# Performance work log

Measured on AMD Instinct MI355X. Metric: run time of the kernel, lower is better.

## Reference

```python
import jax, jax.numpy as jnp
import numpy as np

T, B, D, H, A = 256, 512, 128, 128, 8
RUN_COUNT = 1000

def _orth(k, shape, scale):
    w = jax.random.normal(k, shape, jnp.float32)
    q, r = jnp.linalg.qr(w)
    q = q * jnp.sign(jnp.diag(r))[None, :]
    return scale * q

def setup_inputs() -> dict:
    key = jax.random.key(0)
    ks = jax.random.split(key, 12)
    return {
        'hidden': jnp.zeros((B, H), jnp.float32),
        'obs': jax.random.normal(ks[0], (T, B, D), jnp.float32),
        'dones': (jax.random.randint(ks[1], (T, B), 0, 10) == 0),
        'mean_obs': jax.random.normal(ks[2], (D,), jnp.float32) * 0.1,
        'welford_S': jax.random.uniform(ks[3], (D,), jnp.float32) * RUN_COUNT,
        'running_count': RUN_COUNT,
        'W_emb': _orth(ks[4], (D, H), float(np.sqrt(2.0))), 'b_emb': jnp.zeros((H,), jnp.float32),
        'Wi': jax.random.normal(ks[5], (H, 3 * H), jnp.float32) / np.sqrt(H),
        'Wh': jax.random.normal(ks[6], (H, 3 * H), jnp.float32) / np.sqrt(H),
        'bh': jnp.zeros((3 * H,), jnp.float32),
        'W_act': _orth(ks[7], (H, H), 2.0), 'b_act': jnp.zeros((H,), jnp.float32),
        'W_alpha': _orth(ks[8], (H, A), 0.01), 'b_alpha': jnp.zeros((A,), jnp.float32),
        'W_beta': _orth(ks[9], (H, A), 0.01), 'b_beta': jnp.zeros((A,), jnp.float32),
    }

def _welford(M0, S0, count0, xs):
    # sequential Welford update over stacked rows, as in the original lax.scan
    def step(carry, x):
        M, S, c = carry
        c = c + 1.0
        M_new = M + (x - M) / c
        S_new = S + (x - M) * (x - M_new)
        return (M_new, S_new, c), None
    (M, S, c), _ = jax.lax.scan(step, (M0, S0, jnp.asarray(count0, jnp.float32)), xs)
    return M, S, c

def reference(hidden, obs, dones, mean_obs, welford_S, running_count,
              W_emb, b_emb, Wi, Wh, bh, W_act, b_act, W_alpha, b_alpha, W_beta, b_beta):
    # --- running-stat normalization (running_count > 0 branch) ---
    stacked = obs.reshape(-1, obs.shape[-1])  # [T*B, D]
    M, S, c = _welford(mean_obs, welford_S, running_count, stacked)
    var = S / (c - 1.0)
    obs_n = (obs - M) / (jnp.sqrt(var) + 1e-8)
    # --- embedding MLP ---
    emb = jax.nn.relu(obs_n @ W_emb + b_emb)  # [T, B, H]
    # --- GRU scan over time; precompute input-side gate projections (no input bias, flax GRUCell) ---
    xg = emb @ Wi  # [T, B, 3H]
    def gru_step(h, inp):
        x3, reset = inp
        h = jnp.where(reset[:, None], 0.0, h)  # reset carry where done
        hg = h @ Wh + bh
        xr, xz, xn = jnp.split(x3, 3, axis=-1)
        hr, hz, hn = jnp.split(hg, 3, axis=-1)
        r = jax.nn.sigmoid(xr + hr)
        z = jax.nn.sigmoid(xz + hz)
        n = jnp.tanh(xn + r * hn)
        h_new = (1.0 - z) * n + z * h
        return h_new, h_new
    h_last, ys = jax.lax.scan(gru_step, hidden, (xg, dones))  # ys: [T, B, H]
    # --- policy heads ---
    act = jax.nn.relu(ys @ W_act + b_act)
    alpha = jax.nn.softplus(act @ W_alpha + b_alpha) + 1.0
    beta = jax.nn.softplus(act @ W_beta + b_beta) + 1.0
    return h_last, alpha, beta, M, S
```

## Files before the change

kernel.cpp:

```cpp
#include <hip/hip_runtime.h>

#define T_DIM 256
#define B_DIM 512
#define D_DIM 128
#define H_DIM 128
#define A_DIM 8
#define N_ROWS (T_DIM*B_DIM)
#define NT (N_ROWS/16)
#define NWIN 8
#define WLEN 32
#define LOG2E 1.4426950408889634f

typedef __attribute__((ext_vector_type(4))) float f32x4;
typedef __attribute__((ext_vector_type(8))) short bf16x8;
typedef __attribute__((ext_vector_type(4))) short bf16x4;
typedef __attribute__((ext_vector_type(8))) _Float16 f16x8;
typedef __attribute__((ext_vector_type(4))) unsigned u32x4;
typedef __attribute__((ext_vector_type(2))) unsigned u32x2;

#define OFF_PSUM   0ull
#define OFF_PSQ    1048576ull
#define OFF_STATM  2097152ull
#define OFF_STATI  2097664ull
#define OFF_WEMB   2098176ull
#define OFF_WI     2130944ull
#define OFF_WH     2229248ull
#define OFF_WACT   2425856ull
#define OFF_WHEAD  2458624ull
#define OFF_TLO    2462720ull
#define OFF_UH     2464768ull
#define OFF_XG     4194304ull
#define OFF_YS     104857600ull

#define OUT_H      0
#define OUT_ALPHA  65536
#define OUT_BETA   1114112
#define OUT_M      2162688
#define OUT_S      2162816

__device__ inline short f2bf(float x){
  union { float f; unsigned u; } v; v.f = x;
  unsigned r = v.u + 0x7FFFu + ((v.u>>16)&1u);
  return (short)(r>>16);
}
__device__ inline float bf2f(short h){
  union { unsigned u; float f; } v; v.u = ((unsigned)(unsigned short)h)<<16; return v.f;
}

__device__ inline int swz(int row, int col){ return row*136 + col; }

__device__ inline unsigned cvtpk_bf16(float lo, float hi){
  unsigned r;
  asm("v_cvt_pk_bf16_f32 %0, %1, %2" : "=v"(r) : "v"(lo), "v"(hi));
  return r;
}

__global__ __launch_bounds__(256) void k_partial(const float* __restrict__ obs,
                                                 double* __restrict__ psum,
                                                 double* __restrict__ psq){
  int tid = threadIdx.x; int col = tid & 127; int rh = tid >> 7;
  double s = 0.0, q = 0.0;
  for (int r = blockIdx.x*2 + rh; r < N_ROWS; r += 2048){
    float v = obs[(size_t)r*D_DIM + col];
    s += (double)v; q += (double)v*(double)v;
  }
  __shared__ double ls[256], lq[256];
  ls[tid]=s; lq[tid]=q; __syncthreads();
  if (rh==0){
    psum[(size_t)blockIdx.x*128 + col] = ls[tid] + ls[tid+128];
    psq [(size_t)blockIdx.x*128 + col] = lq[tid] + lq[tid+128];
  }
}

__global__ __launch_bounds__(1024) void k_stats(const double* __restrict__ psum,
                                                const double* __restrict__ psq,
                                                const float* __restrict__ mean_obs,
                                                const float* __restrict__ welfS,
                                                const int* __restrict__ runcnt,
                                                float* __restrict__ outM, float* __restrict__ outS,
                                                float* __restrict__ wsM,  float* __restrict__ wsI){
  int tid = threadIdx.x; int col = tid & 127; int seg = tid >> 7;
  double s=0.0, q=0.0;
  for (int b=seg; b<1024; b+=8){ s += psum[(size_t)b*128+col]; q += psq[(size_t)b*128+col]; }
  __shared__ double ls[1024], lq[1024];
  ls[tid]=s; lq[tid]=q; __syncthreads();
  if (seg==0){
    for (int b=1;b<8;b++){ s += ls[b*128+col]; q += lq[b*128+col]; }
    double c0 = (double)runcnt[0];
    double Nn = (double)N_ROWS;
    double n  = c0 + Nn;
    double M0 = (double)mean_obs[col], S0 = (double)welfS[col];
    double mb = s / Nn;
    double delta = mb - M0;
    double M = M0 + delta * Nn / n;
    double M2b = q - Nn*mb*mb;
    double S = S0 + M2b + delta*delta*c0*Nn/n;
    double var = S / (n - 1.0);
    float inv = (float)(1.0/(sqrt(var)+1e-8));
    outM[col] = (float)M; outS[col] = (float)S;
    wsM[col]  = (float)M; wsI[col]  = inv;
  }
}

__global__ void k_pack_all(const float* __restrict__ W_emb, const float* __restrict__ Wi,
                           const float* __restrict__ Wh,    const float* __restrict__ W_act,
                           const float* __restrict__ W_al,  const float* __restrict__ W_be,
                           short* __restrict__ Bemb, short* __restrict__ BWi,
                           short* __restrict__ BWh,  short* __restrict__ Bact,
                           short* __restrict__ Bhead){
  int gidx = blockIdx.x*256 + threadIdx.x;
  if (gidx >= 133120) return;
  if (gidx >= 131072){
    int idx = gidx - 131072;
    int j = idx & 7, lane = (idx>>3)&63, kb = (idx>>9)&3;
    int k = kb*32 + (lane>>4)*8 + j;
    int n = lane & 15;
    float wv = (n<8) ? W_al[(size_t)k*8 + n] : W_be[(size_t)k*8 + (n-8)];
    Bhead[idx] = f2bf(wv);
    return;
  }
  const float* src; short* dst; int C; int fmt; int idx;
  if (gidx < 16384)      { src=W_emb; dst=Bemb; C=128; fmt=0; idx=gidx; }
  else if (gidx < 65536) { src=Wi;    dst=BWi;  C=384; fmt=0; idx=gidx-16384; }
  else if (gidx < 114688){ src=Wh;    dst=BWh;  C=384; fmt=1; idx=gidx-65536; }
  else                   { src=W_act; dst=Bact; C=128; fmt=0; idx=gidx-114688; }
  int j = idx & 7, lane = (idx>>3)&63, kb = (idx>>9)&3, ct = idx>>11;
  int k = kb*32 + (lane>>4)*8 + j;
  int n = ct*16 + (lane&15);
  float wv = src[(size_t)k*C + n];
  short h;
  if (fmt==0) h = f2bf(wv);
  else {
    wv *= (n < 256) ? LOG2E : (2.f*LOG2E);
    union { _Float16 hf; short s; } u; u.hf = (_Float16)wv; h = u.s;
  }
  dst[idx] = h;
}

__global__ __launch_bounds__(512) void k_sched(const unsigned char* __restrict__ dones,
                                               int* __restrict__ tlo,
                                               unsigned char* __restrict__ usehid){
  int k = blockIdx.x;
  int b = threadIdx.x;
  int t0 = 0, uh = 1;
  if (k > 0){
    for (int t = WLEN*k; t >= 0; t--){
      if (dones[(size_t)t*B_DIM + b]){ t0 = t; uh = 0; break; }
    }
  }
  usehid[k*B_DIM + b] = (unsigned char)uh;
  __shared__ int red[512];
  red[b] = t0; __syncthreads();
  if (b < 32){
    int m = red[b*16];
    #pragma unroll
    for (int i=1;i<16;i++) m = min(m, red[b*16+i]);
    tlo[k*32 + b] = m;
  }
}

__global__ __launch_bounds__(256) void k_embxg(const float* __restrict__ obs,
                                               const float* __restrict__ wsM,
                                               const float* __restrict__ wsI,
                                               const short* __restrict__ Bemb,
                                               const float* __restrict__ b_emb,
                                               const short* __restrict__ BWi,
                                               const float* __restrict__ bh,
                                               short* __restrict__ xgpk){
  int tid=threadIdx.x, w=tid>>6, lane=tid&63, q=lane>>4, l=lane&15;
  __shared__ __align__(16) short Wlds[16384];
  __shared__ __align__(16) short scratch[4][16*136];

  short* Lw = &scratch[w][0];
  int rt0 = blockIdx.x*16 + w*4;

  {
    u32x4* dst = (u32x4*)Wlds;
    const u32x4* src = (const u32x4*)Bemb;
    #pragma unroll
    for (int i=0;i<8;i++) dst[tid + i*256] = src[tid + i*256];
  }
  __syncthreads();

  bf16x8 a2[4][4];
  #pragma unroll
  for (int tt=0; tt<4; tt++){
    int rt = rt0 + tt;
    int r0 = rt*16;
    {
      int row = lane>>2, c0 = (lane&3)*32;
      const float* op = obs + (size_t)(r0+row)*D_DIM + c0;
      #pragma unroll
      for (int it=0; it<8; it++){
        f32x4 o = *(const f32x4*)(op + it*4);
        f32x4 m = *(const f32x4*)(wsM + c0 + it*4);
        f32x4 iv= *(const f32x4*)(wsI + c0 + it*4);
        bf16x4 v;
        v[0]=f2bf((o[0]-m[0])*iv[0]); v[1]=f2bf((o[1]-m[1])*iv[1]);
        v[2]=f2bf((o[2]-m[2])*iv[2]); v[3]=f2bf((o[3]-m[3])*iv[3]);
        *(bf16x4*)&Lw[swz(row, c0+it*4)] = v;
      }
    }
    asm volatile("s_waitcnt lgkmcnt(0)" ::: "memory");
    bf16x8 A[4];
    #pragma unroll
    for (int kb=0;kb<4;kb++) A[kb] = *(const bf16x8*)&Lw[swz(l, kb*32+q*8)];
    asm volatile("s_waitcnt lgkmcnt(0)" ::: "memory");
    #pragma unroll
    for (int ct=0; ct<8; ct++){
      f32x4 acc = {0.f,0.f,0.f,0.f};
      #pragma unroll
      for (int kb=0;kb<4;kb++)
        acc = __builtin_amdgcn_mfma_f32_16x16x32_bf16(A[kb],
                *(const bf16x8*)&Wlds[((ct*4+kb)*64+lane)*8], acc, 0,0,0);
      float bb = b_emb[ct*16 + l];
      #pragma unroll
      for (int r2=0;r2<4;r2++){
        float e = acc[r2] + bb; e = e>0.f ? e : 0.f;
        Lw[swz(q*4+r2, ct*16+l)] = f2bf(e);
      }
    }
    asm volatile("s_waitcnt lgkmcnt(0)" ::: "memory");
    #pragma unroll
    for (int kb=0;kb<4;kb++) a2[tt][kb] = *(const bf16x8*)&Lw[swz(l, kb*32+q*8)];
    asm volatile("s_waitcnt lgkmcnt(0)" ::: "memory");
  }
  __syncthreads();

  u32x2* xg8 = (u32x2*)xgpk;
  for (int g=0; g<3; g++){
    {
      u32x4* dst = (u32x4*)Wlds;
      const u32x4* src = (const u32x4*)BWi + (size_t)g*2048;
      #pragma unroll
      for (int i=0;i<8;i++) dst[tid + i*256] = src[tid + i*256];
    }
    __syncthreads();
    float sc = (g<2) ? LOG2E : (2.f*LOG2E);
    float bb = (g<2) ? bh[g*128 ] : 0.f;
    #pragma unroll
    for (int tt=0; tt<4; tt++){
      int rt = rt0 + tt;
      #pragma unroll
      for (int j=0; j<8; j++){
        int ct = g*8 + j;
        f32x4 acc = {0.f,0.f,0.f,0.f};
        #pragma unroll
        for (int kb=0;kb<4;kb++)
          acc = __builtin_amdgcn_mfma_f32_16x16x32_bf16(a2[tt][kb],
                  *(const bf16x8*)&Wlds[((j*4+kb)*64+lane)*8], acc, 0,0,0);
        int col = ct*16 + l;
        float bv = (g<2) ? bh[col] : 0.f;
        u32x2 pv;
        pv[0] = cvtpk_bf16((acc[0]+bv)*sc, (acc[1]+bv)*sc);
        pv[1] = cvtpk_bf16((acc[2]+bv)*sc, (acc[3]+bv)*sc);
        xg8[((size_t)rt*24 + ct)*64 + lane] = pv;
      }
    }
    if (g < 2) __syncthreads();
    (void)bb;
  }
}

#define LDB(g,kb) __builtin_bit_cast(f16x8, pw4[(((g)*8+w)*4+(kb))*64+lane])
__global__
__attribute__((amdgpu_flat_work_group_size(512,512)))
__attribute__((amdgpu_waves_per_eu(2,2)))
void k_gru(const float* __restrict__ hidden,
           const unsigned char* __restrict__ dones,
           const short* __restrict__ xgpk,
           const short* __restrict__ BWh,
           const float* __restrict__ bh,
           const int* __restrict__ tlo,
           const unsigned char* __restrict__ usehid,
           short* __restrict__ yspk,
           float* __restrict__ h_last){
  int tid=threadIdx.x, w=tid>>6, lane=tid&63, q=lane>>4, l=lane&15;
  int kk = blockIdx.x >> 5, bt = blockIdx.x & 31;
  int t_out0 = kk*WLEN;
  int t_end  = t_out0 + WLEN;
  int t_start = tlo[kk*32 + bt];

  __shared__ __align__(16) _Float16 hF[2][16*136];

  const u32x4* pw4 = (const u32x4*)BWh;
  f16x8 B00 = LDB(0,0), B01 = LDB(0,1), B02 = LDB(0,2), B03 = LDB(0,3);
  f16x8 B10 = LDB(1,0), B11 = LDB(1,1), B12 = LDB(1,2), B13 = LDB(1,3);
  f16x8 B20 = LDB(2,0), B21 = LDB(2,1), B22 = LDB(2,2), B23 = LDB(2,3);

  float bh2c = bh[2*128 + w*16 + l] * (2.f*LOG2E);

  float hv[4];
  #pragma unroll
  for (int r2=0;r2<4;r2++){
    int b = bt*16 + q*4 + r2;
    hv[r2] = usehid[kk*B_DIM + b] ? hidden[(size_t)b*H_DIM + w*16 + l] : 0.f;
  }

  const bf16x4* xgt = (const bf16x4*)xgpk + (((size_t)t_start*32 + bt)*24 + w)*64 + lane;
  const unsigned char* dnp = dones + (size_t)t_start*B_DIM + bt*16 + q*4;
  bf16x4* yst = (bf16x4*)yspk + (((size_t)t_start*32 + bt)*8 + w)*64 + lane;

  bf16x4 xr_c = xgt[0], xz_c = xgt[512], xn_c = xgt[1024];
  unsigned dn_c = *(const unsigned*)dnp;
  { int a1 = (t_start+1 < t_end) ? 1 : 0; xgt += (size_t)a1*49152; dnp += a1*B_DIM; }
  bf16x4 xr_n = xgt[0], xz_n = xgt[512], xn_n = xgt[1024];
  unsigned dn_n = *(const unsigned*)dnp;

  _Float16* hA = &hF[0][0];
  _Float16* hB = &hF[1][0];
  const int wo = q*4*136 + w*16 + l;
  const int ro = l*136 + q*8;

  for (int t = t_start; t < t_end; t++){
    #pragma unroll
    for (int r2=0;r2<4;r2++){
      float hvv = ((dn_c >> (r2*8)) & 255u) ? 0.f : hv[r2];
      hv[r2] = hvv;
      hA[wo + r2*136] = (_Float16)hvv;
    }
    asm volatile("s_waitcnt lgkmcnt(0)" ::: "memory");
    __builtin_amdgcn_s_barrier();
    asm volatile("" ::: "memory");

    int a2 = (t+2 < t_end) ? 1 : 0;
    xgt += (size_t)a2 * 49152;
    dnp += a2 * B_DIM;
    bf16x4 xr_2 = xgt[0], xz_2 = xgt[512], xn_2 = xgt[1024];
    unsigned dn_2 = *(const unsigned*)dnp;

    f16x8 A0 = *(const f16x8*)(hA + ro +  0);
    f16x8 A1 = *(const f16x8*)(hA + ro + 32);
    f16x8 A2 = *(const f16x8*)(hA + ro + 64);
    f16x8 A3 = *(const f16x8*)(hA + ro + 96);

    f32x4 acc0 = {0.f,0.f,0.f,0.f}, acc1 = {0.f,0.f,0.f,0.f}, acc2 = {0.f,0.f,0.f,0.f};
    acc0 = __builtin_amdgcn_mfma_f32_16x16x32_f16(A0, B00, acc0, 0,0,0);
    acc1 = __builtin_amdgcn_mfma_f32_16x16x32_f16(A0, B10, acc1, 0,0,0);
    acc2 = __builtin_amdgcn_mfma_f32_16x16x32_f16(A0, B20, acc2, 0,0,0);
    acc0 = __builtin_amdgcn_mfma_f32_16x16x32_f16(A1, B01, acc0, 0,0,0);
    acc1 = __builtin_amdgcn_mfma_f32_16x16x32_f16(A1, B11, acc1, 0,0,0);
    acc2 = __builtin_amdgcn_mfma_f32_16x16x32_f16(A1, B21, acc2, 0,0,0);
    acc0 = __builtin_amdgcn_mfma_f32_16x16x32_f16(A2, B02, acc0, 0,0,0);
    acc1 = __builtin_amdgcn_mfma_f32_16x16x32_f16(A2, B12, acc1, 0,0,0);
    acc2 = __builtin_amdgcn_mfma_f32_16x16x32_f16(A2, B22, acc2, 0,0,0);
    acc0 = __builtin_amdgcn_mfma_f32_16x16x32_f16(A3, B03, acc0, 0,0,0);
    acc1 = __builtin_amdgcn_mfma_f32_16x16x32_f16(A3, B13, acc1, 0,0,0);
    acc2 = __builtin_amdgcn_mfma_f32_16x16x32_f16(A3, B23, acc2, 0,0,0);

    #pragma unroll
    for (int r2=0;r2<4;r2++){
      float xr = bf2f(xr_c[r2]), xz = bf2f(xz_c[r2]), xn = bf2f(xn_c[r2]);
      float rg = __builtin_amdgcn_rcpf(1.f + __builtin_amdgcn_exp2f(-(xr + acc0[r2])));
      float zg = __builtin_amdgcn_rcpf(1.f + __builtin_amdgcn_exp2f(-(xz + acc1[r2])));
      float e2 = __builtin_amdgcn_exp2f(xn + rg*(acc2[r2] + bh2c));
      float ng = 1.f - 2.f*__builtin_amdgcn_rcpf(e2 + 1.f);
      hv[r2] = ng + zg*(hv[r2] - ng);
    }
    if (t >= t_out0){
      u32x2 pv;
      pv[0] = cvtpk_bf16(hv[0], hv[1]);
      pv[1] = cvtpk_bf16(hv[2], hv[3]);
      *(u32x2*)yst = pv;
    }
    yst += 16384;
    xr_c = xr_n; xz_c = xz_n; xn_c = xn_n; dn_c = dn_n;
    xr_n = xr_2; xz_n = xz_2; xn_n = xn_2; dn_n = dn_2;
    _Float16* tmp = hA; hA = hB; hB = tmp;
  }

  if (kk == NWIN-1){
    #pragma unroll
    for (int r2=0;r2<4;r2++)
      h_last[(size_t)(bt*16+q*4+r2)*H_DIM + w*16 + l] = hv[r2];
  }
}

__global__ __launch_bounds__(256) void k_heads(const short* __restrict__ yspk,
                                               const short* __restrict__ Bact,
                                               const float* __restrict__ b_act,
                                               const short* __restrict__ Bhead,
                                               const float* __restrict__ b_alpha,
                                               const float* __restrict__ b_beta,
                                               float* __restrict__ alpha,
                                               float* __restrict__ beta){
  int tid=threadIdx.x, w=tid>>6, lane=tid&63, q=lane>>4, l=lane&15;
  __shared__ __align__(16) short Wlds[16384];
  __shared__ __align__(16) short Hlds[2048];
  __shared__ __align__(16) short scratch[4][16*136];
  short* Lw = &scratch[w][0];
  size_t rt0 = (size_t)blockIdx.x*16 + w*4;

  {
    u32x4* dst = (u32x4*)Wlds;
    const u32x4* src = (const u32x4*)Bact;
    #pragma unroll
    for (int i=0;i<8;i++) dst[tid + i*256] = src[tid + i*256];
    ((u32x4*)Hlds)[tid] = ((const u32x4*)Bhead)[tid];
  }
  __syncthreads();

  const bf16x4* ys4 = (const bf16x4*)yspk;
  #pragma unroll
  for (int tt=0; tt<4; tt++){
    size_t rt = rt0 + tt;
    #pragma unroll
    for (int ct=0; ct<8; ct++){
      bf16x4 v = ys4[(rt*8+ct)*64+lane];
      #pragma unroll
      for (int r2=0;r2<4;r2++) Lw[swz(q*4+r2, ct*16+l)] = v[r2];
    }
    asm volatile("s_waitcnt lgkmcnt(0)" ::: "memory");
    bf16x8 A[4];
    #pragma unroll
    for (int kb=0;kb<4;kb++) A[kb] = *(const bf16x8*)&Lw[swz(l, kb*32+q*8)];
    asm volatile("s_waitcnt lgkmcnt(0)" ::: "memory");
    #pragma unroll
    for (int ct=0;ct<8;ct++){
      f32x4 acc = {0.f,0.f,0.f,0.f};
      #pragma unroll
      for (int kb=0;kb<4;kb++)
        acc = __builtin_amdgcn_mfma_f32_16x16x32_bf16(A[kb],
                *(const bf16x8*)&Wlds[((ct*4+kb)*64+lane)*8], acc, 0,0,0);
      int col = ct*16 + l;
      float bb = b_act[col];
      #pragma unroll
      for (int r2=0;r2<4;r2++){
        float e = acc[r2] + bb; e = e>0.f ? e : 0.f;
        Lw[swz(q*4+r2, col)] = f2bf(e);
      }
    }
    asm volatile("s_waitcnt lgkmcnt(0)" ::: "memory");
    bf16x8 A2[4];
    #pragma unroll
    for (int kb=0;kb<4;kb++) A2[kb] = *(const bf16x8*)&Lw[swz(l, kb*32+q*8)];
    asm volatile("s_waitcnt lgkmcnt(0)" ::: "memory");
    f32x4 acc = {0.f,0.f,0.f,0.f};
    #pragma unroll
    for (int kb=0;kb<4;kb++)
      acc = __builtin_amdgcn_mfma_f32_16x16x32_bf16(A2[kb],
              *(const bf16x8*)&Hlds[(kb*64+lane)*8], acc, 0,0,0);
    float bb = (l<8) ? b_alpha[l] : b_beta[l-8];
    float* dst = (l<8) ? alpha : beta;
    int cc = (l<8) ? l : l-8;
    #pragma unroll
    for (int r2=0;r2<4;r2++){
      float u = acc[r2] + bb;
      float e = __builtin_amdgcn_exp2f(-fabsf(u)*LOG2E);
      float sp = fmaxf(u,0.f) + 0.6931471805599453f*__builtin_amdgcn_logf(1.f + e);
      dst[(rt*16 + q*4 + r2)*8 + cc] = sp + 1.f;
    }
  }
}

extern "C" void kernel_launch(void* const* d_in, const int* in_sizes, int n_in,
                              void* d_out, int out_size, void* d_ws, size_t ws_size,
                              hipStream_t stream){
  const float* hidden   = (const float*)d_in[0];
  const float* obs      = (const float*)d_in[1];
  const unsigned char* dones = (const unsigned char*)d_in[2];
  const float* mean_obs = (const float*)d_in[3];
  const float* welfS    = (const float*)d_in[4];
  const int*   runcnt   = (const int*)d_in[5];
  const float* W_emb = (const float*)d_in[6];
  const float* b_emb = (const float*)d_in[7];
  const float* Wi    = (const float*)d_in[8];
  const float* Wh    = (const float*)d_in[9];
  const float* bh    = (const float*)d_in[10];
  const float* W_act = (const float*)d_in[11];
  const float* b_act = (const float*)d_in[12];
  const float* W_al  = (const float*)d_in[13];
  const float* b_al  = (const float*)d_in[14];
  const float* W_be  = (const float*)d_in[15];
  const float* b_be  = (const float*)d_in[16];
  float* out = (float*)d_out;
  char*  ws  = (char*)d_ws;

  double* psum = (double*)(ws + OFF_PSUM);
  double* psq  = (double*)(ws + OFF_PSQ);
  float*  wsM  = (float*)(ws + OFF_STATM);
  float*  wsI  = (float*)(ws + OFF_STATI);
  short*  Bemb = (short*)(ws + OFF_WEMB);
  short*  BWi  = (short*)(ws + OFF_WI);
  short*  BWh  = (short*)(ws + OFF_WH);
  short*  Bact = (short*)(ws + OFF_WACT);
  short*  Bhead= (short*)(ws + OFF_WHEAD);
  int*    tlo  = (int*)(ws + OFF_TLO);
  unsigned char* uh = (unsigned char*)(ws + OFF_UH);
  short*  xgpk = (short*)(ws + OFF_XG);
  short*  yspk = (short*)(ws + OFF_YS);

  k_partial<<<1024,256,0,stream>>>(obs, psum, psq);
  k_stats<<<1,1024,0,stream>>>(psum, psq, mean_obs, welfS, runcnt,
                               out+OUT_M, out+OUT_S, wsM, wsI);
  k_sched<<<NWIN,512,0,stream>>>(dones, tlo, uh);
  k_pack_all<<<520,256,0,stream>>>(W_emb, Wi, Wh, W_act, W_al, W_be,
                                   Bemb, BWi, BWh, Bact, Bhead);
  k_embxg<<<512,256,0,stream>>>(obs, wsM, wsI, Bemb, b_emb, BWi, bh, xgpk);
  k_gru<<<NWIN*32,512,0,stream>>>(hidden, dones, xgpk, BWh, bh, tlo, uh,
                                  yspk, out + OUT_H);
  k_heads<<<512,256,0,stream>>>(yspk, Bact, b_act, Bhead, b_al, b_be,
                                out + OUT_ALPHA, out + OUT_BETA);
}
```

Baseline: 502.1 us.

## Fuse stats, schedule and pack kernels; fold policy heads into GRU epilogue

```diff
diff --git a/kernel.cpp b/kernel.cpp
--- a/kernel.cpp
+++ b/kernel.cpp
@@ -55,21 +55,85 @@
   return r;
 }
 
-__global__ __launch_bounds__(256) void k_partial(const float* __restrict__ obs,
-                                                 double* __restrict__ psum,
-                                                 double* __restrict__ psq){
-  int tid = threadIdx.x; int col = tid & 127; int rh = tid >> 7;
-  double s = 0.0, q = 0.0;
-  for (int r = blockIdx.x*2 + rh; r < N_ROWS; r += 2048){
-    float v = obs[(size_t)r*D_DIM + col];
-    s += (double)v; q += (double)v*(double)v;
-  }
+__global__ __launch_bounds__(256)
+void k_fused(const float* __restrict__ obs,
+             double* __restrict__ psum, double* __restrict__ psq,
+             const unsigned char* __restrict__ dones,
+             int* __restrict__ tlo, unsigned char* __restrict__ usehid,
+             const float* __restrict__ W_emb, const float* __restrict__ Wi,
+             const float* __restrict__ Wh,    const float* __restrict__ W_act,
+             const float* __restrict__ W_al,  const float* __restrict__ W_be,
+             short* __restrict__ Bemb, short* __restrict__ BWi,
+             short* __restrict__ BWh,  short* __restrict__ Bact,
+             short* __restrict__ Bhead){
   __shared__ double ls[256], lq[256];
-  ls[tid]=s; lq[tid]=q; __syncthreads();
-  if (rh==0){
-    psum[(size_t)blockIdx.x*128 + col] = ls[tid] + ls[tid+128];
-    psq [(size_t)blockIdx.x*128 + col] = lq[tid] + lq[tid+128];
-  }
+  __shared__ int red[512];
+  int bx = blockIdx.x, tid = threadIdx.x;
+
+  if (bx < 1024){
+    int col = tid & 127; int rh = tid >> 7;
+    double s = 0.0, q = 0.0;
+    for (int r = bx*2 + rh; r < N_ROWS; r += 2048){
+      float v = obs[(size_t)r*D_DIM + col];
+      s += (double)v; q += (double)v*(double)v;
+    }
+    ls[tid]=s; lq[tid]=q; __syncthreads();
+    if (rh==0){
+      psum[(size_t)bx*128 + col] = ls[tid] + ls[tid+128];
+      psq [(size_t)bx*128 + col] = lq[tid] + lq[tid+128];
+    }
+    return;
+  }
+  if (bx < 1032){
+    int k = bx - 1024;
+    #pragma unroll
+    for (int h=0; h<2; h++){
+      int b = tid + h*256;
+      int t0 = 0, uh = 1;
+      if (k > 0){
+        for (int t = WLEN*k; t >= 0; t--){
+          if (dones[(size_t)t*B_DIM + b]){ t0 = t; uh = 0; break; }
+        }
+      }
+      usehid[k*B_DIM + b] = (unsigned char)uh;
+      red[b] = t0;
+    }
+    __syncthreads();
+    if (tid < 32){
+      int m = red[tid*16];
+      #pragma unroll
+      for (int i=1;i<16;i++) m = min(m, red[tid*16+i]);
+      tlo[k*32 + tid] = m;
+    }
+    return;
+  }
+  int gidx = (bx-1032)*256 + tid;
+  if (gidx >= 133120) return;
+  if (gidx >= 131072){
+    int idx = gidx - 131072;
+    int j = idx & 7, lane = (idx>>3)&63, kb = (idx>>9)&3;
+    int k = kb*32 + (lane>>4)*8 + j;
+    int n = lane & 15;
+    float wv = (n<8) ? W_al[(size_t)k*8 + n] : W_be[(size_t)k*8 + (n-8)];
+    Bhead[idx] = f2bf(wv);
+    return;
+  }
+  const float* src; short* dst; int C; int fmt; int idx;
+  if (gidx < 16384)      { src=W_emb; dst=Bemb; C=128; fmt=0; idx=gidx; }
+  else if (gidx < 65536) { src=Wi;    dst=BWi;  C=384; fmt=0; idx=gidx-16384; }
+  else if (gidx < 114688){ src=Wh;    dst=BWh;  C=384; fmt=1; idx=gidx-65536; }
+  else                   { src=W_act; dst=Bact; C=128; fmt=0; idx=gidx-114688; }
+  int j = idx & 7, lane = (idx>>3)&63, kb = (idx>>9)&3, ct = idx>>11;
+  int k = kb*32 + (lane>>4)*8 + j;
+  int n = ct*16 + (lane&15);
+  float wv = src[(size_t)k*C + n];
+  short h;
+  if (fmt==0) h = f2bf(wv);
+  else {
+    wv *= (n < 256) ? LOG2E : (2.f*LOG2E);
+    union { _Float16 hf; short s; } u; u.hf = (_Float16)wv; h = u.s;
+  }
+  dst[idx] = h;
 }
 
 __global__ __launch_bounds__(1024) void k_stats(const double* __restrict__ psum,
@@ -102,63 +166,6 @@
   }
 }
 
-__global__ void k_pack_all(const float* __restrict__ W_emb, const float* __restrict__ Wi,
-                           const float* __restrict__ Wh,    const float* __restrict__ W_act,
-                           const float* __restrict__ W_al,  const float* __restrict__ W_be,
-                           short* __restrict__ Bemb, short* __restrict__ BWi,
-                           short* __restrict__ BWh,  short* __restrict__ Bact,
-                           short* __restrict__ Bhead){
-  int gidx = blockIdx.x*256 + threadIdx.x;
-  if (gidx >= 133120) return;
-  if (gidx >= 131072){
-    int idx = gidx - 131072;
-    int j = idx & 7, lane = (idx>>3)&63, kb = (idx>>9)&3;
-    int k = kb*32 + (lane>>4)*8 + j;
-    int n = lane & 15;
-    float wv = (n<8) ? W_al[(size_t)k*8 + n] : W_be[(size_t)k*8 + (n-8)];
-    Bhead[idx] = f2bf(wv);
-    return;
-  }
-  const float* src; short* dst; int C; int fmt; int idx;
-  if (gidx < 16384)      { src=W_emb; dst=Bemb; C=128; fmt=0; idx=gidx; }
-  else if (gidx < 65536) { src=Wi;    dst=BWi;  C=384; fmt=0; idx=gidx-16384; }
-  else if (gidx < 114688){ src=Wh;    dst=BWh;  C=384; fmt=1; idx=gidx-65536; }
-  else                   { src=W_act; dst=Bact; C=128; fmt=0; idx=gidx-114688; }
-  int j = idx & 7, lane = (idx>>3)&63, kb = (idx>>9)&3, ct = idx>>11;
-  int k = kb*32 + (lane>>4)*8 + j;
-  int n = ct*16 + (lane&15);
-  float wv = src[(size_t)k*C + n];
-  short h;
-  if (fmt==0) h = f2bf(wv);
-  else {
-    wv *= (n < 256) ? LOG2E : (2.f*LOG2E);
-    union { _Float16 hf; short s; } u; u.hf = (_Float16)wv; h = u.s;
-  }
-  dst[idx] = h;
-}
-
-__global__ __launch_bounds__(512) void k_sched(const unsigned char* __restrict__ dones,
-                                               int* __restrict__ tlo,
-                                               unsigned char* __restrict__ usehid){
-  int k = blockIdx.x;
-  int b = threadIdx.x;
-  int t0 = 0, uh = 1;
-  if (k > 0){
-    for (int t = WLEN*k; t >= 0; t--){
-      if (dones[(size_t)t*B_DIM + b]){ t0 = t; uh = 0; break; }
-    }
-  }
-  usehid[k*B_DIM + b] = (unsigned char)uh;
-  __shared__ int red[512];
-  red[b] = t0; __syncthreads();
-  if (b < 32){
-    int m = red[b*16];
-    #pragma unroll
-    for (int i=1;i<16;i++) m = min(m, red[b*16+i]);
-    tlo[k*32 + b] = m;
-  }
-}
-
 __global__ __launch_bounds__(256) void k_embxg(const float* __restrict__ obs,
                                                const float* __restrict__ wsM,
                                                const float* __restrict__ wsI,
@@ -237,7 +244,6 @@
     }
     __syncthreads();
     float sc = (g<2) ? LOG2E : (2.f*LOG2E);
-    float bb = (g<2) ? bh[g*128 ] : 0.f;
     #pragma unroll
     for (int tt=0; tt<4; tt++){
       int rt = rt0 + tt;
@@ -258,7 +264,6 @@
       }
     }
     if (g < 2) __syncthreads();
-    (void)bb;
   }
 }
 
@@ -274,14 +279,21 @@
            const int* __restrict__ tlo,
            const unsigned char* __restrict__ usehid,
            short* __restrict__ yspk,
-           float* __restrict__ h_last){
+           float* __restrict__ h_last,
+           const short* __restrict__ Bact,
+           const float* __restrict__ b_act,
+           const short* __restrict__ Bhead,
+           const float* __restrict__ b_alpha,
+           const float* __restrict__ b_beta,
+           float* __restrict__ alpha,
+           float* __restrict__ beta){
   int tid=threadIdx.x, w=tid>>6, lane=tid&63, q=lane>>4, l=lane&15;
   int kk = blockIdx.x >> 5, bt = blockIdx.x & 31;
   int t_out0 = kk*WLEN;
   int t_end  = t_out0 + WLEN;
   int t_start = tlo[kk*32 + bt];
 
-  __shared__ __align__(16) _Float16 hF[2][16*136];
+  __shared__ __align__(16) char Ubytes[8*16*136*2];
 
   const u32x4* pw4 = (const u32x4*)BWh;
   f16x8 B00 = LDB(0,0), B01 = LDB(0,1), B02 = LDB(0,2), B03 = LDB(0,3);
@@ -307,8 +319,8 @@
   bf16x4 xr_n = xgt[0], xz_n = xgt[512], xn_n = xgt[1024];
   unsigned dn_n = *(const unsigned*)dnp;
 
-  _Float16* hA = &hF[0][0];
-  _Float16* hB = &hF[1][0];
+  _Float16* hA = (_Float16*)Ubytes;
+  _Float16* hB = (_Float16*)Ubytes + 16*136;
   const int wo = q*4*136 + w*16 + l;
   const int ro = l*136 + q*8;
 
@@ -374,36 +386,18 @@
     for (int r2=0;r2<4;r2++)
       h_last[(size_t)(bt*16+q*4+r2)*H_DIM + w*16 + l] = hv[r2];
   }
-}
-
-__global__ __launch_bounds__(256) void k_heads(const short* __restrict__ yspk,
-                                               const short* __restrict__ Bact,
-                                               const float* __restrict__ b_act,
-                                               const short* __restrict__ Bhead,
-                                               const float* __restrict__ b_alpha,
-                                               const float* __restrict__ b_beta,
-                                               float* __restrict__ alpha,
-                                               float* __restrict__ beta){
-  int tid=threadIdx.x, w=tid>>6, lane=tid&63, q=lane>>4, l=lane&15;
-  __shared__ __align__(16) short Wlds[16384];
-  __shared__ __align__(16) short Hlds[2048];
-  __shared__ __align__(16) short scratch[4][16*136];
-  short* Lw = &scratch[w][0];
-  size_t rt0 = (size_t)blockIdx.x*16 + w*4;
-
-  {
-    u32x4* dst = (u32x4*)Wlds;
-    const u32x4* src = (const u32x4*)Bact;
-    #pragma unroll
-    for (int i=0;i<8;i++) dst[tid + i*256] = src[tid + i*256];
-    ((u32x4*)Hlds)[tid] = ((const u32x4*)Bhead)[tid];
-  }
+
+  asm volatile("s_waitcnt vmcnt(0)" ::: "memory");
   __syncthreads();
 
+  short* Lw = (short*)Ubytes + (size_t)w*(16*136);
+  const bf16x8* BA  = (const bf16x8*)Bact;
+  const bf16x8* BHd = (const bf16x8*)Bhead;
   const bf16x4* ys4 = (const bf16x4*)yspk;
-  #pragma unroll
-  for (int tt=0; tt<4; tt++){
-    size_t rt = rt0 + tt;
+
+  for (int j=0; j<4; j++){
+    int t = t_out0 + w*4 + j;
+    size_t rt = (size_t)t*32 + bt;
     #pragma unroll
     for (int ct=0; ct<8; ct++){
       bf16x4 v = ys4[(rt*8+ct)*64+lane];
@@ -420,8 +414,7 @@
       f32x4 acc = {0.f,0.f,0.f,0.f};
       #pragma unroll
       for (int kb=0;kb<4;kb++)
-        acc = __builtin_amdgcn_mfma_f32_16x16x32_bf16(A[kb],
-                *(const bf16x8*)&Wlds[((ct*4+kb)*64+lane)*8], acc, 0,0,0);
+        acc = __builtin_amdgcn_mfma_f32_16x16x32_bf16(A[kb], BA[(ct*4+kb)*64+lane], acc, 0,0,0);
       int col = ct*16 + l;
       float bb = b_act[col];
       #pragma unroll
@@ -438,8 +431,7 @@
     f32x4 acc = {0.f,0.f,0.f,0.f};
     #pragma unroll
     for (int kb=0;kb<4;kb++)
-      acc = __builtin_amdgcn_mfma_f32_16x16x32_bf16(A2[kb],
-              *(const bf16x8*)&Hlds[(kb*64+lane)*8], acc, 0,0,0);
+      acc = __builtin_amdgcn_mfma_f32_16x16x32_bf16(A2[kb], BHd[kb*64+lane], acc, 0,0,0);
     float bb = (l<8) ? b_alpha[l] : b_beta[l-8];
     float* dst = (l<8) ? alpha : beta;
     int cc = (l<8) ? l : l-8;
@@ -490,15 +482,14 @@
   short*  xgpk = (short*)(ws + OFF_XG);
   short*  yspk = (short*)(ws + OFF_YS);
 
-  k_partial<<<1024,256,0,stream>>>(obs, psum, psq);
+  k_fused<<<1552,256,0,stream>>>(obs, psum, psq, dones, tlo, uh,
+                                 W_emb, Wi, Wh, W_act, W_al, W_be,
+                                 Bemb, BWi, BWh, Bact, Bhead);
   k_stats<<<1,1024,0,stream>>>(psum, psq, mean_obs, welfS, runcnt,
                                out+OUT_M, out+OUT_S, wsM, wsI);
-  k_sched<<<NWIN,512,0,stream>>>(dones, tlo, uh);
-  k_pack_all<<<520,256,0,stream>>>(W_emb, Wi, Wh, W_act, W_al, W_be,
-                                   Bemb, BWi, BWh, Bact, Bhead);
   k_embxg<<<512,256,0,stream>>>(obs, wsM, wsI, Bemb, b_emb, BWi, bh, xgpk);
   k_gru<<<NWIN*32,512,0,stream>>>(hidden, dones, xgpk, BWh, bh, tlo, uh,
-                                  yspk, out + OUT_H);
-  k_heads<<<512,256,0,stream>>>(yspk, Bact, b_act, Bhead, b_al, b_be,
-                                out + OUT_ALPHA, out + OUT_BETA);
-}
+                                  yspk, out + OUT_H,
+                                  Bact, b_act, Bhead, b_al, b_be,
+                                  out + OUT_ALPHA, out + OUT_BETA);
+}
```

Measured after the change: 539.1 us. +7.4%, slower.
